# Optimization experiments

Measured on AMD Instinct MI355X. Metric: run time of the kernel, lower is better.

The kernel has to match this reference:

```python
import jax, jax.numpy as jnp
import numpy as np

KERNEL_SIZE = 9  # square structuring element, matches __init__ default
ITERATIONS = 1


def setup_inputs() -> dict:
    key = jax.random.key(0)
    label = jax.random.uniform(key, (16, 1024, 1024, 1), dtype=jnp.float32)
    return {"label": label}


def reference(label):
    # cv2.dilate with np.ones((k,k)) == sliding-window max over a k x k square.
    # Default morphology border value for dilate is -inf, so SAME padding with
    # -inf init reproduces cv2's border behavior exactly.
    out = label
    for _ in range(ITERATIONS):
        out = jax.lax.reduce_window(
            out,
            -jnp.inf,
            jax.lax.max,
            window_dimensions=(1, KERNEL_SIZE, KERNEL_SIZE, 1),
            window_strides=(1, 1, 1, 1),
            padding="SAME",
        )
    # Original layer wraps the result in K.stop_gradient.
    return jax.lax.stop_gradient(out)
```

## Files before the change

### kernel.cpp

```cpp
#include <hip/hip_runtime.h>
#include <math.h>

#define IMG  1024
#define ROWS 16

#define NEG4 make_float4(-INFINITY, -INFINITY, -INFINITY, -INFINITY)

__device__ __forceinline__ float4 max4(const float4 a, const float4 b) {
    return make_float4(fmaxf(a.x, b.x), fmaxf(a.y, b.y),
                       fmaxf(a.z, b.z), fmaxf(a.w, b.w));
}

__device__ __forceinline__ float4 hmax9(const float4 v0, const float4 v1, const float4 v2) {
    const float core = fmaxf(fmaxf(fmaxf(v0.w, v1.x), fmaxf(v1.y, v1.z)),
                             fmaxf(v1.w, v2.x));
    const float p12  = fmaxf(v0.y, v0.z);
    const float q910 = fmaxf(v2.y, v2.z);
    float4 r;
    r.x = fmaxf(core, fmaxf(v0.x, p12));
    r.y = fmaxf(core, fmaxf(p12, v2.y));
    r.z = fmaxf(core, fmaxf(v0.z, q910));
    r.w = fmaxf(core, fmaxf(q910, v2.w));
    return r;
}

__global__ __launch_bounds__(256) void dilate9x9(const float* __restrict__ in,
                                                 float* __restrict__ out) {
    const int x0 = threadIdx.x << 2;
    const int y0 = blockIdx.x * ROWS;
    const int b  = blockIdx.y;

    const float* img  = in  + (size_t)b * IMG * IMG;
    float*       oimg = out + (size_t)b * IMG * IMG;

    const bool hasL = (x0 >= 4);
    const bool hasR = (x0 <= IMG - 8);

    float4 C[8];

    {
        float4 L0[8], L1[8], L2[8];
        bool   val[8];
        #pragma unroll
        for (int j = 0; j < 8; ++j) {
            const int iy = y0 - 4 + j;
            val[j] = (iy >= 0);
            const int cy = val[j] ? iy : 0;
            const float4* p = reinterpret_cast<const float4*>(img + (size_t)cy * IMG + x0);
            L1[j] = p[0];
            L0[j] = *(hasL ? p - 1 : p);
            L2[j] = *(hasR ? p + 1 : p);
        }
        #pragma unroll
        for (int j = 0; j < 8; ++j) {
            const float4 l0 = hasL ? L0[j] : NEG4;
            const float4 l2 = hasR ? L2[j] : NEG4;
            C[j] = val[j] ? hmax9(l0, L1[j], l2) : NEG4;
        }
    }

    #pragma unroll
    for (int c = 0; c < ROWS / 8; ++c) {
        const int r0 = y0 + (c << 3);

        float4 L0[8], L1[8], L2[8];
        bool   val[8];
        #pragma unroll
        for (int j = 0; j < 8; ++j) {
            const int iy = r0 + 4 + j;
            val[j] = (iy < IMG);
            const int cy = val[j] ? iy : IMG - 1;
            const float4* p = reinterpret_cast<const float4*>(img + (size_t)cy * IMG + x0);
            L1[j] = p[0];
            L0[j] = *(hasL ? p - 1 : p);
            L2[j] = *(hasR ? p + 1 : p);
        }

        float4 S[8];
        S[7] = C[7];
        #pragma unroll
        for (int j = 6; j >= 0; --j) S[j] = max4(C[j], S[j + 1]);

        float4 P;
        #pragma unroll
        for (int t = 0; t < 8; ++t) {
            const float4 l0 = hasL ? L0[t] : NEG4;
            const float4 l2 = hasR ? L2[t] : NEG4;
            const float4 H  = val[t] ? hmax9(l0, L1[t], l2) : NEG4;
            P = (t == 0) ? H : max4(P, H);
            *reinterpret_cast<float4*>(oimg + (size_t)(r0 + t) * IMG + x0) = max4(S[t], P);
            C[t] = H;
        }
    }
}

extern "C" void kernel_launch(void* const* d_in, const int* in_sizes, int n_in,
                              void* d_out, int out_size, void* d_ws, size_t ws_size,
                              hipStream_t stream) {
    const float* in  = (const float*)d_in[0];
    float*       out = (float*)d_out;
    const int B = in_sizes[0] / (IMG * IMG);
    dim3 grid(IMG / ROWS, B);
    dilate9x9<<<grid, 256, 0, stream>>>(in, out);
}
```

Before: 31.25 us.

## Stage input rows in a double-buffered LDS ring via async global-to-LDS loads

Replaces the per-thread triple global float4 loads (left, centre and right neighbours) with one async global_load_lds per row into a two-slot shared-memory ring. Each block now covers 32 rows and prefetches the next 8 rows while it computes the current chunk, synchronised with manual vmcnt waits and barriers. The intent is to cut redundant global/L2 traffic from the horizontal halo and to overlap loads with compute. In exchange it uses 64KB of LDS per block and halves the block count, which lowers occupancy and parallelism. The hand-written vmcnt accounting also depends on how loads and stores are counted and ordered.

```diff
diff --git a/kernel.cpp b/kernel.cpp
--- a/kernel.cpp
+++ b/kernel.cpp
@@ -2,7 +2,7 @@
 #include <math.h>
 
 #define IMG  1024
-#define ROWS 16
+#define ROWS 32
 
 #define NEG4 make_float4(-INFINITY, -INFINITY, -INFINITY, -INFINITY)
 
@@ -24,58 +24,70 @@
     return r;
 }
 
-__global__ __launch_bounds__(256) void dilate9x9(const float* __restrict__ in,
-                                                 float* __restrict__ out) {
-    const int x0 = threadIdx.x << 2;
-    const int y0 = blockIdx.x * ROWS;
-    const int b  = blockIdx.y;
+__global__ __launch_bounds__(256, 1)
+void dilate9x9(const float* __restrict__ in, float* __restrict__ out) {
+    __shared__ float ring[2][8][IMG];
+
+    const int tid = threadIdx.x;
+    const int w   = tid >> 6;
+    const int ln  = tid & 63;
+    const int x4  = tid << 2;
+    const int y0  = blockIdx.x * ROWS;
+    const int b   = blockIdx.y;
 
     const float* img  = in  + (size_t)b * IMG * IMG;
     float*       oimg = out + (size_t)b * IMG * IMG;
 
-    const bool hasL = (x0 >= 4);
-    const bool hasR = (x0 <= IMG - 8);
+    auto stage = [&](const int slot, const int r, const int cy) {
+        const float* gsrc = img + (size_t)cy * IMG + (w << 8) + (ln << 2);
+        float* lptr = &ring[slot][r][w << 8];
+        __builtin_amdgcn_global_load_lds(
+            (const __attribute__((address_space(1))) void*)gsrc,
+            (__attribute__((address_space(3))) void*)lptr,
+            16, 0, 0);
+    };
+
+    auto hrow = [&](const float* row) -> float4 {
+        const float4 v1 = *reinterpret_cast<const float4*>(&row[x4]);
+        const float4 v0 = (tid == 0)   ? NEG4
+                        : *reinterpret_cast<const float4*>(&row[x4 - 4]);
+        const float4 v2 = (tid == 255) ? NEG4
+                        : *reinterpret_cast<const float4*>(&row[x4 + 4]);
+        return hmax9(v0, v1, v2);
+    };
+
+    #pragma unroll
+    for (int j = 0; j < 8; ++j) {
+        const int iy = y0 - 4 + j;
+        stage(0, j, iy >= 0 ? iy : 0);
+    }
+    #pragma unroll
+    for (int j = 0; j < 8; ++j) {
+        const int iy = y0 + 4 + j;
+        stage(1, j, iy < IMG ? iy : IMG - 1);
+    }
+    asm volatile("s_waitcnt vmcnt(8)" ::: "memory");
+    __builtin_amdgcn_s_barrier();
 
     float4 C[8];
-
-    {
-        float4 L0[8], L1[8], L2[8];
-        bool   val[8];
-        #pragma unroll
-        for (int j = 0; j < 8; ++j) {
-            const int iy = y0 - 4 + j;
-            val[j] = (iy >= 0);
-            const int cy = val[j] ? iy : 0;
-            const float4* p = reinterpret_cast<const float4*>(img + (size_t)cy * IMG + x0);
-            L1[j] = p[0];
-            L0[j] = *(hasL ? p - 1 : p);
-            L2[j] = *(hasR ? p + 1 : p);
-        }
-        #pragma unroll
-        for (int j = 0; j < 8; ++j) {
-            const float4 l0 = hasL ? L0[j] : NEG4;
-            const float4 l2 = hasR ? L2[j] : NEG4;
-            C[j] = val[j] ? hmax9(l0, L1[j], l2) : NEG4;
-        }
-    }
+    #pragma unroll
+    for (int j = 0; j < 8; ++j)
+        C[j] = (y0 - 4 + j >= 0) ? hrow(ring[0][j]) : NEG4;
 
     #pragma unroll
-    for (int c = 0; c < ROWS / 8; ++c) {
-        const int r0 = y0 + (c << 3);
-
-        float4 L0[8], L1[8], L2[8];
-        bool   val[8];
-        #pragma unroll
-        for (int j = 0; j < 8; ++j) {
-            const int iy = r0 + 4 + j;
-            val[j] = (iy < IMG);
-            const int cy = val[j] ? iy : IMG - 1;
-            const float4* p = reinterpret_cast<const float4*>(img + (size_t)cy * IMG + x0);
-            L1[j] = p[0];
-            L0[j] = *(hasL ? p - 1 : p);
-            L2[j] = *(hasR ? p + 1 : p);
+    for (int c = 0; c < 4; ++c) {
+        if (c == 0) asm volatile("s_waitcnt vmcnt(0)" ::: "memory");
+        else        asm volatile("s_waitcnt vmcnt(8)" ::: "memory");
+        __builtin_amdgcn_s_barrier();
+        if (c < 3) {
+            #pragma unroll
+            for (int j = 0; j < 8; ++j) {
+                const int iy = y0 + 12 + (c << 3) + j;
+                stage(c & 1, j, iy < IMG ? iy : IMG - 1);
+            }
         }
 
+        const int r0 = y0 + (c << 3);
         float4 S[8];
         S[7] = C[7];
         #pragma unroll
@@ -84,11 +96,9 @@
         float4 P;
         #pragma unroll
         for (int t = 0; t < 8; ++t) {
-            const float4 l0 = hasL ? L0[t] : NEG4;
-            const float4 l2 = hasR ? L2[t] : NEG4;
-            const float4 H  = val[t] ? hmax9(l0, L1[t], l2) : NEG4;
+            const float4 H = (r0 + 4 + t < IMG) ? hrow(ring[(c + 1) & 1][t]) : NEG4;
             P = (t == 0) ? H : max4(P, H);
-            *reinterpret_cast<float4*>(oimg + (size_t)(r0 + t) * IMG + x0) = max4(S[t], P);
+            *reinterpret_cast<float4*>(oimg + (size_t)(r0 + t) * IMG + x4) = max4(S[t], P);
             C[t] = H;
         }
     }
```

Result: no change. 30.85 us (-1.3%).
